# Kernel optimization log

Measured on AMD Instinct MI355X. Metric: run time of the kernel, lower is better.

The kernel has to match this reference:

```python
import jax, jax.numpy as jnp
import numpy as np

HEADS = 8
HEAD_DIM = 32
DIM = 256        # embed_dim; inner_dim = HEADS*HEAD_DIM = 256
DEPTH = 2
MLP_DIM = 1024
GRID_H, GRID_W = 64, 64
CELL_DIM = 15    # pe(0) + in(3) + out(3) + hidden(9)
PE_IN = 3        # cell_pe_patch_dim + cell_in_patch_dim
UPDATE_DIM = 12  # cell_out(3) + hidden(9)
BATCH = 8


def layer_norm(x, g, b, eps=1e-5):
    m = jnp.mean(x, axis=-1, keepdims=True)
    v = jnp.var(x, axis=-1, keepdims=True)
    return (x - m) * jax.lax.rsqrt(v + eps) * g + b


def vit_positional_encoding(n, dim):
    pos = jnp.arange(n, dtype=jnp.float32)[:, None]
    div = jnp.exp(jnp.arange(0, dim, 2, dtype=jnp.float32) * (-np.log(10000.0) / dim))
    pe = jnp.zeros((n, dim), dtype=jnp.float32)
    pe = pe.at[:, 0::2].set(jnp.sin(pos * div)).at[:, 1::2].set(jnp.cos(pos * div))
    return pe[None]  # [1, n, dim]


def localize(x, H, W):
    # x: [b, heads, n, d] with n = H*W. Gather circular 3x3 neighbourhood per position
    # (equivalent to circular pad + one-hot conv in the torch LocalizeAttention).
    b, nh, n, d = x.shape
    y = x.reshape(b, nh, H, W, d)
    neigh = [jnp.roll(y, (1 - ki, 1 - kj), axis=(2, 3)) for ki in range(3) for kj in range(3)]
    return jnp.stack(neigh, axis=4).reshape(b, nh, n, 9, d)  # [b, h, n, 9, d]


def setup_inputs() -> dict:
    key = jax.random.key(0)
    ks = jax.random.split(key, 20)
    d = {}
    d['cells'] = jax.random.normal(ks[0], (BATCH, CELL_DIM, GRID_H, GRID_W), dtype=jnp.float32)
    s = 0.02
    d['We'] = jax.random.normal(ks[1], (CELL_DIM, DIM), jnp.float32) * s
    d['be'] = jnp.zeros((DIM,), jnp.float32)
    d['ln1_g'] = jnp.ones((DEPTH, DIM), jnp.float32)
    d['ln1_b'] = jnp.zeros((DEPTH, DIM), jnp.float32)
    d['Wqkv'] = jax.random.normal(ks[2], (DEPTH, DIM, 3 * HEADS * HEAD_DIM), jnp.float32) * s
    d['Wo'] = jax.random.normal(ks[3], (DEPTH, HEADS * HEAD_DIM, DIM), jnp.float32) * s
    d['bo'] = jnp.zeros((DEPTH, DIM), jnp.float32)
    d['ln2_g'] = jnp.ones((DEPTH, DIM), jnp.float32)
    d['ln2_b'] = jnp.zeros((DEPTH, DIM), jnp.float32)
    d['W1'] = jax.random.normal(ks[4], (DEPTH, DIM, MLP_DIM), jnp.float32) * s
    d['b1'] = jnp.zeros((DEPTH, MLP_DIM), jnp.float32)
    d['W2'] = jax.random.normal(ks[5], (DEPTH, MLP_DIM, DIM), jnp.float32) * s
    d['b2'] = jnp.zeros((DEPTH, DIM), jnp.float32)
    d['lnh_g'] = jnp.ones((DIM,), jnp.float32)
    d['lnh_b'] = jnp.zeros((DIM,), jnp.float32)
    # NOTE: torch zero-inits mlp_head; we use small random weights so the output is nontrivial.
    d['Wh'] = jax.random.normal(ks[6], (DIM, UPDATE_DIM), jnp.float32) * s
    d['bh'] = jnp.zeros((UPDATE_DIM,), jnp.float32)
    return d


def reference(cells, We, be, ln1_g, ln1_b, Wqkv, Wo, bo, ln2_g, ln2_b,
              W1, b1, W2, b2, lnh_g, lnh_b, Wh, bh):
    b, c, H, W = cells.shape
    n = H * W
    x = cells.reshape(b, c, n).transpose(0, 2, 1)           # b n c
    x = x @ We + be                                         # cell_to_embedding
    x = x + vit_positional_encoding(n, x.shape[-1])
    scale = HEAD_DIM ** -0.5
    for l in range(DEPTH):
        y = layer_norm(x, ln1_g[l], ln1_b[l])
        qkv = y @ Wqkv[l]                                   # b n 3*inner
        q, k, v = jnp.split(qkv, 3, axis=-1)
        split_heads = lambda t: t.reshape(b, n, HEADS, HEAD_DIM).transpose(0, 2, 1, 3)
        q, k, v = split_heads(q), split_heads(k), split_heads(v)  # b h n d
        kl = localize(k, H, W)                              # b h n 9 d
        vl = localize(v, H, W)
        dots = jnp.einsum('bhnd,bhnkd->bhnk', q, kl) * scale
        attn = jax.nn.softmax(dots, axis=-1)
        out = jnp.einsum('bhnk,bhnkd->bhnd', attn, vl)
        out = out.transpose(0, 2, 1, 3).reshape(b, n, HEADS * HEAD_DIM)
        x = out @ Wo[l] + bo[l] + x                         # attention + residual
        y = layer_norm(x, ln2_g[l], ln2_b[l])
        y = jax.nn.gelu(y @ W1[l] + b1[l], approximate=False) @ W2[l] + b2[l]
        x = x + y                                           # ffn + residual
    upd = layer_norm(x, lnh_g, lnh_b) @ Wh + bh             # b n UPDATE_DIM
    upd = upd.transpose(0, 2, 1).reshape(b, UPDATE_DIM, H, W)
    # update_rate = 1.0 -> deterministic branch: cells[:, PE_IN:] + update
    updated = cells[:, PE_IN:] + upd
    return jnp.concatenate([cells[:, :PE_IN], updated], axis=1)
```

## Files before the change

kernel.cpp:

```cpp
#include <hip/hip_runtime.h>
#include <hip/hip_bf16.h>
#include <math.h>

#define HEADS 8
#define HEAD_DIM 32
#define DIM 256
#define MLP_DIM 1024
#define NTOK 4096
#define BATCH 8
#define M_TOK (BATCH*NTOK)
#define CELL_DIM 15
#define PE_IN 3
#define UPD 12
#define HME ((size_t)M_TOK*32)

typedef __attribute__((ext_vector_type(8))) short bf16x8;
typedef __attribute__((ext_vector_type(4))) float f32x4;

static __device__ __forceinline__ unsigned short f2bf(float f) {
    __hip_bfloat16 h = __float2bfloat16(f);
    union { __hip_bfloat16 h; unsigned short u; } cv; cv.h = h; return cv.u;
}
static __device__ __forceinline__ void gload_lds16(const unsigned short* g, unsigned short* l) {
    __builtin_amdgcn_global_load_lds(
        (const __attribute__((address_space(1))) void*)g,
        (__attribute__((address_space(3))) void*)l, 16, 0, 0);
}
static __device__ __forceinline__ float gelu_fast(float v) {
    return v / (1.f + __expf(-1.59576912f * (v + 0.044715f * v * v * v)));
}

__global__ __launch_bounds__(256) void k_embed(const float* __restrict__ cells,
        const float* __restrict__ We, const float* __restrict__ be,
        const float* __restrict__ g, const float* __restrict__ bln,
        float* __restrict__ x, unsigned short* __restrict__ y) {
    __shared__ float red[8];
    int tok = blockIdx.x;
    int d = threadIdx.x;
    int b = tok >> 12, n = tok & 4095;
    const float* cb = cells + (size_t)b * CELL_DIM * NTOK + n;
    float acc = 0.f;
#pragma unroll
    for (int c = 0; c < CELL_DIM; ++c)
        acc += cb[c * NTOK] * We[c * DIM + d];
    int i = d >> 1;
    float freq = expf(-logf(10000.f) * (float)(2 * i) / (float)DIM);
    float ph = (float)n * freq;
    float pe = (d & 1) ? cosf(ph) : sinf(ph);
    float v = acc + be[d] + pe;
    x[(size_t)tok * DIM + d] = v;
    float s = v, ss = v * v;
#pragma unroll
    for (int off = 32; off; off >>= 1) { s += __shfl_xor(s, off); ss += __shfl_xor(ss, off); }
    int wave = d >> 6, lane = d & 63;
    if (lane == 0) { red[wave] = s; red[4 + wave] = ss; }
    __syncthreads();
    float stot = red[0] + red[1] + red[2] + red[3];
    float sstot = red[4] + red[5] + red[6] + red[7];
    float mean = stot * (1.f / DIM);
    float rstd = rsqrtf(sstot * (1.f / DIM) - mean * mean + 1e-5f);
    y[(size_t)tok * DIM + d] = f2bf((v - mean) * rstd * g[d] + bln[d]);
}

__global__ __launch_bounds__(256) void k_prep(const float* __restrict__ Wqkv,
        const float* __restrict__ Wo, const float* __restrict__ W1,
        const float* __restrict__ W2, const float* __restrict__ Wh,
        unsigned short* __restrict__ wT) {
    int seg = blockIdx.y;
    int idx = blockIdx.x * 256 + threadIdx.x;
    if (seg == 8) {
        if (idx >= 16 * 256) return;
        int u = idx >> 8, k = idx & 255;
        wT[1572864 + idx] = (u < UPD) ? f2bf(Wh[(size_t)k * UPD + u]) : (unsigned short)0;
        return;
    }
    int l = seg >> 2, mat = seg & 3;
    const float* src; int kwSh, Nw; size_t ooff;
    switch (mat) {
        case 0: src = Wqkv + (size_t)l * 196608; kwSh = 8;  Nw = 768;  ooff = (size_t)l * 786432 + 0;      break;
        case 1: src = Wo   + (size_t)l * 65536;  kwSh = 8;  Nw = 256;  ooff = (size_t)l * 786432 + 196608; break;
        case 2: src = W1   + (size_t)l * 262144; kwSh = 8;  Nw = 1024; ooff = (size_t)l * 786432 + 262144; break;
        default:src = W2   + (size_t)l * 262144; kwSh = 10; Nw = 256;  ooff = (size_t)l * 786432 + 524288; break;
    }
    int Kw = 1 << kwSh;
    if (idx >= Kw * Nw) return;
    int n = idx >> kwSh, k = idx & (Kw - 1);
    wT[ooff + idx] = f2bf(src[(size_t)k * Nw + n]);
}

template<int EPI>
__global__ __launch_bounds__(256) void k_mgemm(const unsigned short* __restrict__ A,
        const unsigned short* __restrict__ BT, const float* __restrict__ bias,
        void* __restrict__ Cout, int M, int N, int K, int NT) {
    __shared__ unsigned short As[3][128 * 32];
    __shared__ unsigned short Bs[3][128 * 32];
    int bid = blockIdx.x;
    int cpx = gridDim.x >> 3;
    int sb = (bid & 7) * cpx + (bid >> 3);
    int mt = sb / NT, nt = sb - mt * NT;
    int m0 = mt * 128, n0 = nt * 128;
    int t = threadIdx.x;
    int lane = t & 63, w = t >> 6;
    int wm = (w >> 1) * 64, wn = (w & 1) * 64;
    f32x4 acc[4][4] = {};
    int srow = t >> 2;
    int cg = (t & 3) ^ ((srow >> 1) & 3);
    const unsigned short* aBase = A  + (size_t)(m0 + srow) * K + cg * 8;
    const unsigned short* bBase = BT + (size_t)(n0 + srow) * K + cg * 8;
    int fr = lane & 15, kb8 = lane >> 4;

    auto stage = [&](int buf, int k0) {
        unsigned short* a = &As[0][0] + buf * 4096;
        unsigned short* b = &Bs[0][0] + buf * 4096;
        gload_lds16(aBase + k0,          a + t * 8);
        gload_lds16(aBase + 64 * K + k0, a + 2048 + t * 8);
        gload_lds16(bBase + k0,          b + t * 8);
        gload_lds16(bBase + 64 * K + k0, b + 2048 + t * 8);
    };
    auto compute = [&](int buf) {
        const unsigned short* a = &As[0][0] + buf * 4096;
        const unsigned short* b = &Bs[0][0] + buf * 4096;
        bf16x8 af[4], bfv[4];
#pragma unroll
        for (int i = 0; i < 4; ++i) {
            int r_ = wm + i * 16 + fr;
            af[i] = *(const bf16x8*)&a[r_ * 32 + ((kb8 ^ ((r_ >> 1) & 3)) << 3)];
        }
#pragma unroll
        for (int j = 0; j < 4; ++j) {
            int r_ = wn + j * 16 + fr;
            bfv[j] = *(const bf16x8*)&b[r_ * 32 + ((kb8 ^ ((r_ >> 1) & 3)) << 3)];
        }
#pragma unroll
        for (int i = 0; i < 4; ++i)
#pragma unroll
            for (int j = 0; j < 4; ++j)
                acc[i][j] = __builtin_amdgcn_mfma_f32_16x16x32_bf16(bfv[j], af[i], acc[i][j], 0, 0, 0);
    };

    int nk = K >> 5;
    stage(0, 0);
    stage(1, 32);
    asm volatile("s_waitcnt vmcnt(4)" ::: "memory");
    __builtin_amdgcn_s_barrier();
    __builtin_amdgcn_sched_barrier(0);
    int cur = 0;
    for (int k = 0; k < nk - 1; ++k) {
        int pre = k + 2;
        if (pre < nk) {
            int preBuf = cur + 2; if (preBuf >= 3) preBuf -= 3;
            stage(preBuf, pre * 32);
        }
        compute(cur);
        __builtin_amdgcn_sched_barrier(0);
        if (pre < nk) asm volatile("s_waitcnt vmcnt(4)" ::: "memory");
        else          asm volatile("s_waitcnt vmcnt(0)" ::: "memory");
        __builtin_amdgcn_s_barrier();
        __builtin_amdgcn_sched_barrier(0);
        ++cur; if (cur >= 3) cur -= 3;
    }
    compute(cur);

    int mcol = lane & 15, nq = (lane >> 4) * 4;
#pragma unroll
    for (int i = 0; i < 4; ++i) {
        int m = m0 + wm + i * 16 + mcol;
#pragma unroll
        for (int j = 0; j < 4; ++j) {
            int ng = n0 + wn + j * 16 + nq;
            if (EPI == 3) {
                int type = ng >> 8, rem = ng & 255;
                ushort4 pk;
                pk.x = f2bf(acc[i][j][0]); pk.y = f2bf(acc[i][j][1]);
                pk.z = f2bf(acc[i][j][2]); pk.w = f2bf(acc[i][j][3]);
                *(ushort4*)((unsigned short*)Cout +
                    (size_t)(type * 8 + (rem >> 5)) * HME + (size_t)m * 32 + (rem & 31)) = pk;
            } else {
                float4 b4 = *(const float4*)&bias[ng];
                ushort4 pk;
                pk.x = f2bf(gelu_fast(acc[i][j][0] + b4.x));
                pk.y = f2bf(gelu_fast(acc[i][j][1] + b4.y));
                pk.z = f2bf(gelu_fast(acc[i][j][2] + b4.z));
                pk.w = f2bf(gelu_fast(acc[i][j][3] + b4.w));
                *(ushort4*)((unsigned short*)Cout + (size_t)m * N + ng) = pk;
            }
        }
    }
}

template<int ALAYOUT>
__global__ __launch_bounds__(512) void k_mgemm_ln(const unsigned short* __restrict__ A,
        const unsigned short* __restrict__ BT, const float* __restrict__ bias,
        const float* __restrict__ g, const float* __restrict__ bln,
        float* __restrict__ x, unsigned short* __restrict__ y, int K) {
    __shared__ unsigned short As[3][128 * 32];
    __shared__ unsigned short Bs[3][256 * 32];
    __shared__ float sred[128 * 4];
    __shared__ float ssred[128 * 4];
    __shared__ float msr[128 * 2];
    int t = threadIdx.x;
    int lane = t & 63, w = t >> 6;
    int wm = (w >> 2) * 64, wn = (w & 3) * 64, wnq = w & 3;
    int m0 = blockIdx.x * 128;

    f32x4 acc[4][4] = {};
    int srow = t >> 2;
    int cg = (t & 3) ^ ((srow >> 1) & 3);
    const unsigned short* aBase = (ALAYOUT == 0)
        ? A + (size_t)(m0 + srow) * K + cg * 8
        : A + (size_t)(m0 + srow) * 32 + cg * 8;
    const unsigned short* bBase = BT + (size_t)srow * K + cg * 8;
    int fr = lane & 15, kb8 = lane >> 4;

    auto stage = [&](int buf, int k0) {
        unsigned short* as_ = &As[0][0] + buf * 4096;
        unsigned short* bs_ = &Bs[0][0] + buf * 8192;
        const unsigned short* aSrc = (ALAYOUT == 0) ? aBase + k0 : aBase + (size_t)(k0 >> 5) * HME;
        gload_lds16(aSrc,                 as_ + t * 8);
        gload_lds16(bBase + k0,           bs_ + t * 8);
        gload_lds16(bBase + 128 * K + k0, bs_ + 4096 + t * 8);
    };
    auto compute = [&](int buf) {
        const unsigned short* as_ = &As[0][0] + buf * 4096;
        const unsigned short* bs_ = &Bs[0][0] + buf * 8192;
        bf16x8 af[4], bfv[4];
#pragma unroll
        for (int i = 0; i < 4; ++i) {
            int r_ = wm + i * 16 + fr;
            af[i] = *(const bf16x8*)&as_[r_ * 32 + ((kb8 ^ ((r_ >> 1) & 3)) << 3)];
        }
#pragma unroll
        for (int j = 0; j < 4; ++j) {
            int r_ = wn + j * 16 + fr;
            bfv[j] = *(const bf16x8*)&bs_[r_ * 32 + ((kb8 ^ ((r_ >> 1) & 3)) << 3)];
        }
#pragma unroll
        for (int i = 0; i < 4; ++i)
#pragma unroll
            for (int j = 0; j < 4; ++j)
                acc[i][j] = __builtin_amdgcn_mfma_f32_16x16x32_bf16(bfv[j], af[i], acc[i][j], 0, 0, 0);
    };

    int nk = K >> 5;
    stage(0, 0);
    stage(1, 32);
    asm volatile("s_waitcnt vmcnt(3)" ::: "memory");
    __builtin_amdgcn_s_barrier();
    __builtin_amdgcn_sched_barrier(0);
    int cur = 0;
    for (int k = 0; k < nk - 1; ++k) {
        int pre = k + 2;
        if (pre < nk) {
            int preBuf = cur + 2; if (preBuf >= 3) preBuf -= 3;
            stage(preBuf, pre * 32);
        }
        compute(cur);
        __builtin_amdgcn_sched_barrier(0);
        if (pre < nk) asm volatile("s_waitcnt vmcnt(3)" ::: "memory");
        else          asm volatile("s_waitcnt vmcnt(0)" ::: "memory");
        __builtin_amdgcn_s_barrier();
        __builtin_amdgcn_sched_barrier(0);
        ++cur; if (cur >= 3) cur -= 3;
    }
    compute(cur);

    int mloc = lane & 15, nq = (lane >> 4) * 4;
#pragma unroll
    for (int i = 0; i < 4; ++i) {
        int gm = m0 + wm + i * 16 + mloc;
        float s = 0.f, ss = 0.f;
#pragma unroll
        for (int j = 0; j < 4; ++j) {
            int nb = wn + j * 16 + nq;
            float4 b4 = *(const float4*)&bias[nb];
            float4 x4 = *(const float4*)&x[(size_t)gm * DIM + nb];
            acc[i][j][0] += b4.x + x4.x;
            acc[i][j][1] += b4.y + x4.y;
            acc[i][j][2] += b4.z + x4.z;
            acc[i][j][3] += b4.w + x4.w;
#pragma unroll
            for (int r = 0; r < 4; ++r) { float v = acc[i][j][r]; s += v; ss += v * v; }
        }
        s += __shfl_xor(s, 16); ss += __shfl_xor(ss, 16);
        s += __shfl_xor(s, 32); ss += __shfl_xor(ss, 32);
        if (lane < 16) {
            int row = wm + i * 16 + lane;
            sred[row * 4 + wnq] = s;
            ssred[row * 4 + wnq] = ss;
        }
    }
    __syncthreads();
    if (t < 128) {
        float s = sred[t * 4] + sred[t * 4 + 1] + sred[t * 4 + 2] + sred[t * 4 + 3];
        float ss = ssred[t * 4] + ssred[t * 4 + 1] + ssred[t * 4 + 2] + ssred[t * 4 + 3];
        float mean = s * (1.f / DIM);
        float var = ss * (1.f / DIM) - mean * mean;
        msr[t * 2] = mean;
        msr[t * 2 + 1] = rsqrtf(var + 1e-5f);
    }
    __syncthreads();
#pragma unroll
    for (int i = 0; i < 4; ++i) {
        int row = wm + i * 16 + mloc;
        int gm = m0 + row;
        float mean = msr[row * 2], rstd = msr[row * 2 + 1];
#pragma unroll
        for (int j = 0; j < 4; ++j) {
            int nb = wn + j * 16 + nq;
            float4 gv4 = *(const float4*)&g[nb];
            float4 bb4 = *(const float4*)&bln[nb];
            float4 xo;
            xo.x = acc[i][j][0]; xo.y = acc[i][j][1];
            xo.z = acc[i][j][2]; xo.w = acc[i][j][3];
            *(float4*)&x[(size_t)gm * DIM + nb] = xo;
            ushort4 yv;
            yv.x = f2bf((xo.x - mean) * rstd * gv4.x + bb4.x);
            yv.y = f2bf((xo.y - mean) * rstd * gv4.y + bb4.y);
            yv.z = f2bf((xo.z - mean) * rstd * gv4.z + bb4.z);
            yv.w = f2bf((xo.w - mean) * rstd * gv4.w + bb4.w);
            *(ushort4*)&y[(size_t)gm * DIM + nb] = yv;
        }
    }
}

__global__ __launch_bounds__(256) void k_attn(const unsigned short* __restrict__ qkvH,
        unsigned short* __restrict__ attnH) {
    int t = threadIdx.x;
    int h = t >> 5, tl = t & 31;
    int tok = blockIdx.x * 32 + tl;
    int b = tok >> 12, n = tok & 4095;
    int r = n >> 6, c = n & 63;

    float q[32];
    {
        const uint4* u = (const uint4*)(qkvH + (size_t)h * HME + (size_t)tok * 32);
#pragma unroll
        for (int i = 0; i < 4; ++i) {
            uint4 x4 = u[i];
            unsigned wv[4] = {x4.x, x4.y, x4.z, x4.w};
#pragma unroll
            for (int wj = 0; wj < 4; ++wj) {
                q[i * 8 + wj * 2]     = __uint_as_float(wv[wj] << 16);
                q[i * 8 + wj * 2 + 1] = __uint_as_float(wv[wj] & 0xffff0000u);
            }
        }
    }
    int nts[9];
    float dots[9];
    const unsigned short* kbase = qkvH + (size_t)(8 + h) * HME;
#pragma unroll
    for (int ki = 0; ki < 3; ++ki)
#pragma unroll
        for (int kj = 0; kj < 3; ++kj) {
            int rr = (r + ki - 1) & 63, cc = (c + kj - 1) & 63;
            int nt = (b << 12) + (rr << 6) + cc;
            nts[ki * 3 + kj] = nt;
            const uint4* u = (const uint4*)(kbase + (size_t)nt * 32);
            float acc = 0.f;
#pragma unroll
            for (int i = 0; i < 4; ++i) {
                uint4 x4 = u[i];
                unsigned wv[4] = {x4.x, x4.y, x4.z, x4.w};
#pragma unroll
                for (int wj = 0; wj < 4; ++wj) {
                    acc += __uint_as_float(wv[wj] << 16)        * q[i * 8 + wj * 2];
                    acc += __uint_as_float(wv[wj] & 0xffff0000u) * q[i * 8 + wj * 2 + 1];
                }
            }
            dots[ki * 3 + kj] = acc * 0.17677669529f;
        }
    float m = dots[0];
#pragma unroll
    for (int j = 1; j < 9; ++j) m = fmaxf(m, dots[j]);
    float sum = 0.f;
#pragma unroll
    for (int j = 0; j < 9; ++j) { dots[j] = __expf(dots[j] - m); sum += dots[j]; }
    float inv = 1.f / sum;
    float o[32] = {};
    const unsigned short* vbase = qkvH + (size_t)(16 + h) * HME;
#pragma unroll
    for (int j = 0; j < 9; ++j) {
        float wgt = dots[j] * inv;
        const uint4* u = (const uint4*)(vbase + (size_t)nts[j] * 32);
#pragma unroll
        for (int i = 0; i < 4; ++i) {
            uint4 x4 = u[i];
            unsigned wv[4] = {x4.x, x4.y, x4.z, x4.w};
#pragma unroll
            for (int wj = 0; wj < 4; ++wj) {
                o[i * 8 + wj * 2]     += wgt * __uint_as_float(wv[wj] << 16);
                o[i * 8 + wj * 2 + 1] += wgt * __uint_as_float(wv[wj] & 0xffff0000u);
            }
        }
    }
    uint4 st[4];
    unsigned* sw = (unsigned*)st;
#pragma unroll
    for (int i = 0; i < 16; ++i)
        sw[i] = (unsigned)f2bf(o[2 * i]) | ((unsigned)f2bf(o[2 * i + 1]) << 16);
    uint4* od = (uint4*)(attnH + (size_t)h * HME + (size_t)tok * 32);
#pragma unroll
    for (int i = 0; i < 4; ++i) od[i] = st[i];
}

__global__ __launch_bounds__(256) void k_headgemv(const unsigned short* __restrict__ y,
        const unsigned short* __restrict__ WhT, float* __restrict__ Cg) {
    int t = threadIdx.x, lane = t & 63, w = t >> 6;
    int m0 = blockIdx.x * 64 + w * 16;
    int fr = lane & 15, kb = (lane >> 4) * 8;
    f32x4 acc = {};
    const unsigned short* aRow = y + (size_t)(m0 + fr) * DIM + kb;
    const unsigned short* bRow = WhT + (size_t)fr * DIM + kb;
#pragma unroll
    for (int k0 = 0; k0 < DIM; k0 += 32) {
        bf16x8 a = *(const bf16x8*)(aRow + k0);
        bf16x8 bfr = *(const bf16x8*)(bRow + k0);
        acc = __builtin_amdgcn_mfma_f32_16x16x32_bf16(a, bfr, acc, 0, 0, 0);
    }
    int col = lane & 15, rowq = (lane >> 4) * 4;
#pragma unroll
    for (int r = 0; r < 4; ++r)
        Cg[(size_t)(m0 + rowq + r) * 16 + col] = acc[r];
}

__global__ __launch_bounds__(256) void k_assemble(const float* __restrict__ cells,
        const float* __restrict__ Cg, const float* __restrict__ bh,
        float* __restrict__ outp) {
    int idx = blockIdx.x * 256 + threadIdx.x;
    int total = BATCH * CELL_DIM * (NTOK / 4);
    if (idx >= total) return;
    int n4 = idx & 1023;
    int c = (idx >> 10) % CELL_DIM;
    int b = idx / (CELL_DIM * 1024);
    size_t ci = ((size_t)b * CELL_DIM + c) * NTOK + n4 * 4;
    float4 o = *(const float4*)(cells + ci);
    if (c >= PE_IN) {
        int u = c - PE_IN;
        float bias = bh[u];
        size_t tok = (size_t)b * NTOK + n4 * 4;
        o.x += Cg[(tok + 0) * 16 + u] + bias;
        o.y += Cg[(tok + 1) * 16 + u] + bias;
        o.z += Cg[(tok + 2) * 16 + u] + bias;
        o.w += Cg[(tok + 3) * 16 + u] + bias;
    }
    *(float4*)(outp + ci) = o;
}

extern "C" void kernel_launch(void* const* d_in, const int* in_sizes, int n_in,
                              void* d_out, int out_size, void* d_ws, size_t ws_size,
                              hipStream_t stream) {
    const float* cells = (const float*)d_in[0];
    const float* We    = (const float*)d_in[1];
    const float* be    = (const float*)d_in[2];
    const float* ln1_g = (const float*)d_in[3];
    const float* ln1_b = (const float*)d_in[4];
    const float* Wqkv  = (const float*)d_in[5];
    const float* Wo    = (const float*)d_in[6];
    const float* bo    = (const float*)d_in[7];
    const float* ln2_g = (const float*)d_in[8];
    const float* ln2_b = (const float*)d_in[9];
    const float* W1    = (const float*)d_in[10];
    const float* b1    = (const float*)d_in[11];
    const float* W2    = (const float*)d_in[12];
    const float* b2    = (const float*)d_in[13];
    const float* lnh_g = (const float*)d_in[14];
    const float* lnh_b = (const float*)d_in[15];
    const float* Wh    = (const float*)d_in[16];
    const float* bh    = (const float*)d_in[17];
    float* outp = (float*)d_out;

    char* ws = (char*)d_ws;
    float* x = (float*)ws;
    unsigned short* y = (unsigned short*)(ws + 33554432);
    unsigned short* scratch = (unsigned short*)(ws + 50331648);
    unsigned short* wT = (unsigned short*)(ws + 117440512);
    unsigned short* qkvH  = scratch;
    unsigned short* attnH = scratch + 24 * HME;
    unsigned short* hidden = scratch;
    float* Cg = (float*)scratch;

    k_prep<<<dim3(1024, 9), 256, 0, stream>>>(Wqkv, Wo, W1, W2, Wh, wT);
    k_embed<<<M_TOK, 256, 0, stream>>>(cells, We, be, ln1_g, ln1_b, x, y);
    for (int l = 0; l < 2; ++l) {
        const unsigned short* wL = wT + (size_t)l * 786432;
        const float* gN = (l == 0) ? ln1_g + DIM : lnh_g;
        const float* bN = (l == 0) ? ln1_b + DIM : lnh_b;
        k_mgemm<3><<<1536, 256, 0, stream>>>(
            y, wL + 0, nullptr, qkvH, M_TOK, 768, DIM, 6);
        k_attn<<<M_TOK / 32, 256, 0, stream>>>(qkvH, attnH);
        k_mgemm_ln<1><<<M_TOK / 128, 512, 0, stream>>>(
            attnH, wL + 196608, bo + l * DIM, ln2_g + l * DIM, ln2_b + l * DIM, x, y, DIM);
        k_mgemm<1><<<2048, 256, 0, stream>>>(
            y, wL + 262144, b1 + l * MLP_DIM, hidden, M_TOK, MLP_DIM, DIM, 8);
        k_mgemm_ln<0><<<M_TOK / 128, 512, 0, stream>>>(
            hidden, wL + 524288, b2 + l * DIM, gN, bN, x, y, MLP_DIM);
    }
    k_headgemv<<<M_TOK / 64, 256, 0, stream>>>(y, wT + 1572864, Cg);
    k_assemble<<<(BATCH * CELL_DIM * (NTOK / 4) + 255) / 256, 256, 0, stream>>>(cells, Cg, bh, outp);
}
```

Before: 387.4 us.

## Shrink LN-fused GEMM tile to 64 rows, prefetch residual early, fast PE math

```diff
diff --git a/kernel.cpp b/kernel.cpp
--- a/kernel.cpp
+++ b/kernel.cpp
@@ -44,9 +44,9 @@
     for (int c = 0; c < CELL_DIM; ++c)
         acc += cb[c * NTOK] * We[c * DIM + d];
     int i = d >> 1;
-    float freq = expf(-logf(10000.f) * (float)(2 * i) / (float)DIM);
+    float freq = __expf(-0.03597789f * (float)(2 * i));
     float ph = (float)n * freq;
-    float pe = (d & 1) ? cosf(ph) : sinf(ph);
+    float pe = (d & 1) ? __cosf(ph) : __sinf(ph);
     float v = acc + be[d] + pe;
     x[(size_t)tok * DIM + d] = v;
     float s = v, ss = v * v;
@@ -189,19 +189,30 @@
 }
 
 template<int ALAYOUT>
-__global__ __launch_bounds__(512) void k_mgemm_ln(const unsigned short* __restrict__ A,
+__global__ __launch_bounds__(256, 2) void k_mgemm_ln(const unsigned short* __restrict__ A,
         const unsigned short* __restrict__ BT, const float* __restrict__ bias,
         const float* __restrict__ g, const float* __restrict__ bln,
         float* __restrict__ x, unsigned short* __restrict__ y, int K) {
-    __shared__ unsigned short As[3][128 * 32];
+    __shared__ unsigned short As[3][64 * 32];
     __shared__ unsigned short Bs[3][256 * 32];
-    __shared__ float sred[128 * 4];
-    __shared__ float ssred[128 * 4];
-    __shared__ float msr[128 * 2];
+    __shared__ float sred[64 * 4];
+    __shared__ float ssred[64 * 4];
+    __shared__ float msr[64 * 2];
     int t = threadIdx.x;
     int lane = t & 63, w = t >> 6;
-    int wm = (w >> 2) * 64, wn = (w & 3) * 64, wnq = w & 3;
-    int m0 = blockIdx.x * 128;
+    int wn = w * 64;
+    int m0 = blockIdx.x * 64;
+    int mloc = lane & 15, nq = (lane >> 4) * 4;
+
+    float4 xres[4][4];
+#pragma unroll
+    for (int i = 0; i < 4; ++i) {
+        int gm = m0 + i * 16 + mloc;
+#pragma unroll
+        for (int j = 0; j < 4; ++j)
+            xres[i][j] = *(const float4*)&x[(size_t)gm * DIM + wn + j * 16 + nq];
+    }
+    __builtin_amdgcn_sched_barrier(0);
 
     f32x4 acc[4][4] = {};
     int srow = t >> 2;
@@ -213,26 +224,27 @@
     int fr = lane & 15, kb8 = lane >> 4;
 
     auto stage = [&](int buf, int k0) {
-        unsigned short* as_ = &As[0][0] + buf * 4096;
+        unsigned short* as_ = &As[0][0] + buf * 2048;
         unsigned short* bs_ = &Bs[0][0] + buf * 8192;
         const unsigned short* aSrc = (ALAYOUT == 0) ? aBase + k0 : aBase + (size_t)(k0 >> 5) * HME;
-        gload_lds16(aSrc,                 as_ + t * 8);
-        gload_lds16(bBase + k0,           bs_ + t * 8);
-        gload_lds16(bBase + 128 * K + k0, bs_ + 4096 + t * 8);
+        gload_lds16(aSrc, as_ + t * 8);
+#pragma unroll
+        for (int i = 0; i < 4; ++i)
+            gload_lds16(bBase + (size_t)(64 * i) * K + k0, bs_ + i * 2048 + t * 8);
     };
     auto compute = [&](int buf) {
-        const unsigned short* as_ = &As[0][0] + buf * 4096;
-        const unsigned short* bs_ = &Bs[0][0] + buf * 8192;
+        const unsigned short* as_ = &As[0][0] + buf * 2048;
+        const unsigned short* bs_ = &Bs[0][0] + buf * 8192 + w * 2048;
         bf16x8 af[4], bfv[4];
 #pragma unroll
         for (int i = 0; i < 4; ++i) {
-            int r_ = wm + i * 16 + fr;
+            int r_ = i * 16 + fr;
             af[i] = *(const bf16x8*)&as_[r_ * 32 + ((kb8 ^ ((r_ >> 1) & 3)) << 3)];
         }
 #pragma unroll
         for (int j = 0; j < 4; ++j) {
-            int r_ = wn + j * 16 + fr;
-            bfv[j] = *(const bf16x8*)&bs_[r_ * 32 + ((kb8 ^ ((r_ >> 1) & 3)) << 3)];
+            int rl = j * 16 + fr;
+            bfv[j] = *(const bf16x8*)&bs_[rl * 32 + ((kb8 ^ ((rl >> 1) & 3)) << 3)];
         }
 #pragma unroll
         for (int i = 0; i < 4; ++i)
@@ -244,7 +256,7 @@
     int nk = K >> 5;
     stage(0, 0);
     stage(1, 32);
-    asm volatile("s_waitcnt vmcnt(3)" ::: "memory");
+    asm volatile("s_waitcnt vmcnt(5)" ::: "memory");
     __builtin_amdgcn_s_barrier();
     __builtin_amdgcn_sched_barrier(0);
     int cur = 0;
@@ -256,7 +268,7 @@
         }
         compute(cur);
         __builtin_amdgcn_sched_barrier(0);
-        if (pre < nk) asm volatile("s_waitcnt vmcnt(3)" ::: "memory");
+        if (pre < nk) asm volatile("s_waitcnt vmcnt(5)" ::: "memory");
         else          asm volatile("s_waitcnt vmcnt(0)" ::: "memory");
         __builtin_amdgcn_s_barrier();
         __builtin_amdgcn_sched_barrier(0);
@@ -264,33 +276,30 @@
     }
     compute(cur);
 
-    int mloc = lane & 15, nq = (lane >> 4) * 4;
 #pragma unroll
     for (int i = 0; i < 4; ++i) {
-        int gm = m0 + wm + i * 16 + mloc;
         float s = 0.f, ss = 0.f;
 #pragma unroll
         for (int j = 0; j < 4; ++j) {
             int nb = wn + j * 16 + nq;
             float4 b4 = *(const float4*)&bias[nb];
-            float4 x4 = *(const float4*)&x[(size_t)gm * DIM + nb];
-            acc[i][j][0] += b4.x + x4.x;
-            acc[i][j][1] += b4.y + x4.y;
-            acc[i][j][2] += b4.z + x4.z;
-            acc[i][j][3] += b4.w + x4.w;
+            acc[i][j][0] += b4.x + xres[i][j].x;
+            acc[i][j][1] += b4.y + xres[i][j].y;
+            acc[i][j][2] += b4.z + xres[i][j].z;
+            acc[i][j][3] += b4.w + xres[i][j].w;
 #pragma unroll
             for (int r = 0; r < 4; ++r) { float v = acc[i][j][r]; s += v; ss += v * v; }
         }
         s += __shfl_xor(s, 16); ss += __shfl_xor(ss, 16);
         s += __shfl_xor(s, 32); ss += __shfl_xor(ss, 32);
         if (lane < 16) {
-            int row = wm + i * 16 + lane;
-            sred[row * 4 + wnq] = s;
-            ssred[row * 4 + wnq] = ss;
+            int row = i * 16 + lane;
+            sred[row * 4 + w] = s;
+            ssred[row * 4 + w] = ss;
         }
     }
     __syncthreads();
-    if (t < 128) {
+    if (t < 64) {
         float s = sred[t * 4] + sred[t * 4 + 1] + sred[t * 4 + 2] + sred[t * 4 + 3];
         float ss = ssred[t * 4] + ssred[t * 4 + 1] + ssred[t * 4 + 2] + ssred[t * 4 + 3];
         float mean = s * (1.f / DIM);
@@ -301,7 +310,7 @@
     __syncthreads();
 #pragma unroll
     for (int i = 0; i < 4; ++i) {
-        int row = wm + i * 16 + mloc;
+        int row = i * 16 + mloc;
         int gm = m0 + row;
         float mean = msr[row * 2], rstd = msr[row * 2 + 1];
 #pragma unroll
@@ -488,11 +497,11 @@
         k_mgemm<3><<<1536, 256, 0, stream>>>(
             y, wL + 0, nullptr, qkvH, M_TOK, 768, DIM, 6);
         k_attn<<<M_TOK / 32, 256, 0, stream>>>(qkvH, attnH);
-        k_mgemm_ln<1><<<M_TOK / 128, 512, 0, stream>>>(
+        k_mgemm_ln<1><<<M_TOK / 64, 256, 0, stream>>>(
             attnH, wL + 196608, bo + l * DIM, ln2_g + l * DIM, ln2_b + l * DIM, x, y, DIM);
         k_mgemm<1><<<2048, 256, 0, stream>>>(
             y, wL + 262144, b1 + l * MLP_DIM, hidden, M_TOK, MLP_DIM, DIM, 8);
-        k_mgemm_ln<0><<<M_TOK / 128, 512, 0, stream>>>(
+        k_mgemm_ln<0><<<M_TOK / 64, 256, 0, stream>>>(
             hidden, wL + 524288, b2 + l * DIM, gN, bN, x, y, MLP_DIM);
     }
     k_headgemv<<<M_TOK / 64, 256, 0, stream>>>(y, wT + 1572864, Cg);
```

Result: no change. 382.6 us (-1.2%).
